# Kernel tuning notes

Hardware: AMD Instinct MI355X
Metric: run time of the kernel (lower is better)

The kernel has to match this reference:

```python
import jax, jax.numpy as jnp
import numpy as np

B, N, D, H, E = 4, 1024, 1024, 2048, 8

def setup_inputs() -> dict:
    key = jax.random.key(0)
    ks = jax.random.split(key, 5)
    return {
        "x": jax.random.normal(ks[0], (B, N, D), dtype=jnp.float32),
        "gate_w": jax.random.normal(ks[1], (D, E), dtype=jnp.float32) * 0.02,
        "gate_b": jnp.zeros((E,), dtype=jnp.float32),
        "w1": jax.random.normal(ks[2], (E, D, H), dtype=jnp.float32) * 0.02,
        "b1": jnp.zeros((E, H), dtype=jnp.float32),
        "w2": jax.random.normal(ks[3], (E, H, D), dtype=jnp.float32) * 0.02,
        "b2": jnp.zeros((E, D), dtype=jnp.float32),
        "gamma": jnp.ones((D,), dtype=jnp.float32),
    }

def reference(x, gate_w, gate_b, w1, b1, w2, b2, gamma):
    b, n, d = x.shape
    e = w1.shape[0]
    xf = x.reshape(b * n, d)                                    # [T, D]
    # gate: softmax over experts, then top-1
    probs = jax.nn.softmax(xf @ gate_w + gate_b, axis=-1)       # [T, E]
    top_val = jnp.max(probs, axis=-1, keepdims=True)            # [T, 1]
    top_idx = jnp.argmax(probs, axis=-1)                        # [T]
    # all-expert FFN (dense reference for masked dispatch; dropout in eval)
    h = jax.nn.gelu(jnp.einsum('td,edh->eth', xf, w1) + b1[:, None, :],
                    approximate=False)                          # [E, T, H]
    eo = jnp.einsum('eth,ehd->etd', h, w2) + b2[:, None, :]     # [E, T, D]
    onehot = jax.nn.one_hot(top_idx, e, dtype=xf.dtype)         # [T, E]
    out = jnp.einsum('etd,te->td', eo, onehot)                  # select routed expert
    y = (xf + out * top_val).reshape(b, n, d)
    # RMSNorm: F.normalize (L2, eps=1e-12) * gamma * sqrt(dim)
    nrm = jnp.linalg.norm(y, axis=-1, keepdims=True)
    y = y / jnp.maximum(nrm, 1e-12) * gamma * np.float32(np.sqrt(d))
    # load-balancing loss (unbiased variance like torch.var)
    importance = probs.sum(axis=0)                              # [E]
    load_loss = jnp.var(importance, ddof=1) / (jnp.mean(importance) ** 2 + 1e-10)
    return jax.nn.gelu(y, approximate=False), load_loss
```

## Files before the change

### kernel.cpp

```cpp
#include <hip/hip_runtime.h>
#include <math.h>

#define T_TOK 4096
#define DIM   1024
#define HID   2048
#define NE    8
#define TMM   128
#define BK    64
#define GATE_BLOCKS (T_TOK / 4)

typedef unsigned int  u32;
typedef unsigned short u16;
typedef __attribute__((ext_vector_type(8))) short bf16x8;
typedef __attribute__((ext_vector_type(8))) unsigned short u16x8;
typedef __attribute__((ext_vector_type(4))) float f32x4;

__device__ __forceinline__ float gelu_exact(float v) {
    return 0.5f * v * (1.0f + erff(v * 0.70710678118654752440f));
}

__device__ __forceinline__ float gelu_fast(float x) {
    float u = 1.5957691216057308f * (x + 0.044715f * x * x * x);
    float e = __expf(u);
    float t = 1.f - 2.f / (e + 1.f);
    return 0.5f * x * (1.f + t);
}

__device__ __forceinline__ u16 f2bf(float v) {
    u32 u = __float_as_uint(v);
    u32 r = (u + 0x7FFFu + ((u >> 16) & 1u)) >> 16;
    return (u16)r;
}

__device__ __forceinline__ void gld_lds16(const void* g, void* l) {
    __builtin_amdgcn_global_load_lds(
        (const __attribute__((address_space(1))) u32*)g,
        (__attribute__((address_space(3))) u32*)l,
        16, 0, 0);
}

__device__ __forceinline__ void transpose_body(
    const float* __restrict__ in, u16* __restrict__ out, int R, int C,
    int bx, int by, int bz, float (*tile)[65])
{
    const float* src = in  + (size_t)bz * R * C;
    u16*         dst = out + (size_t)bz * R * C;
    const int c0 = bx * 64, r0 = by * 64;
    const int th = threadIdx.x;

    const int tr  = th >> 4;
    const int tc4 = (th & 15) * 4;
    #pragma unroll
    for (int i = 0; i < 4; i++) {
        const int r = tr + i * 16;
        float4 v = *(const float4*)&src[(size_t)(r0 + r) * C + c0 + tc4];
        tile[r][tc4 + 0] = v.x; tile[r][tc4 + 1] = v.y;
        tile[r][tc4 + 2] = v.z; tile[r][tc4 + 3] = v.w;
    }
    __syncthreads();
    const int cc  = th >> 3;
    const int rr8 = (th & 7) * 8;
    #pragma unroll
    for (int i = 0; i < 2; i++) {
        const int c = cc + i * 32;
        u16x8 o;
        #pragma unroll
        for (int j = 0; j < 8; j++) o[j] = f2bf(tile[rr8 + j][c]);
        *(u16x8*)&dst[(size_t)(c0 + c) * R + r0 + rr8] = o;
    }
}

__global__ __launch_bounds__(256) void prep_kernel(
    const float* __restrict__ w1, const float* __restrict__ w2,
    u16* __restrict__ w1t, u16* __restrict__ w2t,
    const float* __restrict__ x, const float* __restrict__ gw,
    const float* __restrict__ gb, float* __restrict__ top_val,
    int* __restrict__ top_idx, float* __restrict__ partial_imp,
    int* __restrict__ partial_cnt)
{
    __shared__ float tile[64][65];
    __shared__ float s_imp[NE];
    __shared__ int   s_cnt[NE];

    const int id = blockIdx.x;
    if (id < 4096) {
        transpose_body(w1, w1t, DIM, HID, id & 31, (id >> 5) & 15, id >> 9, tile);
        return;
    }
    if (id < 8192) {
        const int i2 = id - 4096;
        transpose_body(w2, w2t, HID, DIM, i2 & 15, (i2 >> 4) & 31, i2 >> 9, tile);
        return;
    }

    const int g = id - 8192;
    const int th = threadIdx.x;
    if (th < NE) { s_imp[th] = 0.f; s_cnt[th] = 0; }
    __syncthreads();

    const int wave = th >> 6;
    const int lane = th & 63;
    const int t = g * 4 + wave;

    float acc[NE];
    #pragma unroll
    for (int e = 0; e < NE; e++) acc[e] = 0.f;

    const float* xr = x + (size_t)t * DIM;
    #pragma unroll 4
    for (int k = lane; k < DIM; k += 64) {
        float xv = xr[k];
        const float* gp = gw + (size_t)k * NE;
        float4 g0 = *(const float4*)gp;
        float4 g1 = *(const float4*)(gp + 4);
        acc[0] += xv * g0.x; acc[1] += xv * g0.y;
        acc[2] += xv * g0.z; acc[3] += xv * g0.w;
        acc[4] += xv * g1.x; acc[5] += xv * g1.y;
        acc[6] += xv * g1.z; acc[7] += xv * g1.w;
    }
    #pragma unroll
    for (int e = 0; e < NE; e++) {
        #pragma unroll
        for (int off = 32; off > 0; off >>= 1)
            acc[e] += __shfl_down(acc[e], off, 64);
    }
    if (lane == 0) {
        float l[NE];
        float m = -1e30f;
        #pragma unroll
        for (int e = 0; e < NE; e++) { l[e] = acc[e] + gb[e]; m = fmaxf(m, l[e]); }
        float s = 0.f;
        #pragma unroll
        for (int e = 0; e < NE; e++) { l[e] = expf(l[e] - m); s += l[e]; }
        float inv = 1.f / s;
        int bi = 0; float bv = -1.f;
        #pragma unroll
        for (int e = 0; e < NE; e++) {
            float p = l[e] * inv;
            atomicAdd(&s_imp[e], p);
            if (p > bv) { bv = p; bi = e; }
        }
        top_val[t] = bv;
        top_idx[t] = bi;
        atomicAdd(&s_cnt[bi], 1);
    }
    __syncthreads();
    if (th < NE) {
        partial_imp[g * NE + th] = s_imp[th];
        partial_cnt[g * NE + th] = s_cnt[th];
    }
}

__global__ __launch_bounds__(256) void route_kernel(
    const float* __restrict__ partial_imp, const int* __restrict__ partial_cnt,
    const int* __restrict__ top_idx,
    int* __restrict__ sorted_tok,
    int* __restrict__ tile_e, int* __restrict__ tile_s,
    int* __restrict__ tile_rows, int* __restrict__ ntiles,
    float* __restrict__ loss_out)
{
    __shared__ float rimp[32][NE];
    __shared__ int   rcnt[32][NE];
    __shared__ int   s_off[NE];
    __shared__ int   s_cur[NE];
    const int th = threadIdx.x;
    const int e = th & 7, chunk = th >> 3;
    float si = 0.f; int sc = 0;
    #pragma unroll 8
    for (int i = 0; i < GATE_BLOCKS / 32; i++) {
        const int b = chunk * (GATE_BLOCKS / 32) + i;
        si += partial_imp[b * NE + e];
        sc += partial_cnt[b * NE + e];
    }
    rimp[chunk][e] = si;
    rcnt[chunk][e] = sc;
    __syncthreads();
    if (th < NE) {
        float s = 0.f; int c = 0;
        for (int i = 0; i < 32; i++) { s += rimp[i][th]; c += rcnt[i][th]; }
        rimp[0][th] = s;
        rcnt[0][th] = c;
        s_cur[th] = 0;
    }
    __syncthreads();
    if (th == 0) {
        int off = 0, nt = 0;
        for (int ee = 0; ee < NE; ee++) {
            s_off[ee] = off;
            const int c = rcnt[0][ee];
            for (int s = 0; s < c; s += TMM) {
                tile_e[nt] = ee;
                tile_s[nt] = off + s;
                tile_rows[nt] = min(TMM, c - s);
                nt++;
            }
            off += c;
        }
        *ntiles = nt;

        float mean = 0.f;
        for (int ee = 0; ee < NE; ee++) mean += rimp[0][ee];
        mean *= (1.0f / NE);
        float var = 0.f;
        for (int ee = 0; ee < NE; ee++) { float d = rimp[0][ee] - mean; var += d * d; }
        var *= (1.0f / (NE - 1));
        loss_out[0] = var / (mean * mean + 1e-10f);
    }
    __syncthreads();
    #pragma unroll 4
    for (int r = 0; r < T_TOK / 256; r++) {
        const int t  = r * 256 + th;
        const int te = top_idx[t];
        const int rank = atomicAdd(&s_cur[te], 1);
        sorted_tok[s_off[te] + rank] = t;
    }
}

__global__ __launch_bounds__(256) void gather_x_kernel(
    const float* __restrict__ x, const int* __restrict__ sorted_tok,
    u16* __restrict__ xs)
{
    const int s = blockIdx.x;
    const int tok = sorted_tok[s];
    const float* src = x + (size_t)tok * DIM;
    u16* dst = xs + (size_t)s * DIM;
    const int i = threadIdx.x * 4;
    float4 v = *(const float4*)&src[i];
    ushort4 o;
    o.x = f2bf(v.x); o.y = f2bf(v.y); o.z = f2bf(v.z); o.w = f2bf(v.w);
    *(ushort4*)&dst[i] = o;
}

__global__ __launch_bounds__(512) void ffn1_mfma(
    const u16* __restrict__ xs, const u16* __restrict__ w1t,
    const float* __restrict__ b1,
    const int* __restrict__ tile_e, const int* __restrict__ tile_s,
    const int* __restrict__ tile_rows, const int* __restrict__ ntiles,
    u16* __restrict__ h_buf)
{
    const int tile = blockIdx.x;
    if (tile >= *ntiles) return;
    const int e     = tile_e[tile];
    const int sbase = tile_s[tile];
    const int rows  = tile_rows[tile];
    const int nbase = blockIdx.y * 256;

    __shared__ __align__(16) u16 As[128 * BK];
    __shared__ __align__(16) u16 Bs[256 * BK];

    const int th = threadIdx.x;
    const int w  = th >> 6;
    const int l  = th & 63;
    const int wm = w >> 2, wn = w & 3;
    const int lr = l >> 3;
    const int lcs = ((l & 7) ^ lr) * 8;

    const u16* aptr[2];
    #pragma unroll
    for (int c = 0; c < 2; c++) {
        int srow = sbase + c * 64 + w * 8 + lr;
        if (srow > T_TOK - 1) srow = T_TOK - 1;
        aptr[c] = xs + (size_t)srow * DIM + lcs;
    }
    const u16* wb = w1t + (size_t)e * HID * DIM + (size_t)nbase * DIM;
    const u16* bptr[4];
    #pragma unroll
    for (int c = 0; c < 4; c++)
        bptr[c] = wb + (size_t)(c * 64 + w * 8 + lr) * DIM + lcs;

    f32x4 acc[4][4] = {};

    for (int k0 = 0; k0 < DIM; k0 += BK) {
        __syncthreads();
        #pragma unroll
        for (int c = 0; c < 2; c++)
            gld_lds16(aptr[c] + k0, &As[(c * 64 + w * 8) * BK]);
        #pragma unroll
        for (int c = 0; c < 4; c++)
            gld_lds16(bptr[c] + k0, &Bs[(c * 64 + w * 8) * BK]);
        __syncthreads();
        #pragma unroll
        for (int ks = 0; ks < 2; ks++) {
            const int ko = ((ks * 4 + (l >> 4)) ^ (l & 7)) * 8;
            bf16x8 af[4], bfr[4];
            #pragma unroll
            for (int i = 0; i < 4; i++)
                af[i]  = *(const bf16x8*)&As[(wm * 64 + i * 16 + (l & 15)) * BK + ko];
            #pragma unroll
            for (int i = 0; i < 4; i++)
                bfr[i] = *(const bf16x8*)&Bs[(wn * 64 + i * 16 + (l & 15)) * BK + ko];
            #pragma unroll
            for (int mi = 0; mi < 4; mi++)
                #pragma unroll
                for (int ni = 0; ni < 4; ni++)
                    acc[mi][ni] = __builtin_amdgcn_mfma_f32_16x16x32_bf16(
                        af[mi], bfr[ni], acc[mi][ni], 0, 0, 0);
        }
    }

    const int col = l & 15, quad = l >> 4;
    #pragma unroll
    for (int ni = 0; ni < 4; ni++) {
        const int n = nbase + wn * 64 + ni * 16 + col;
        const float bias = b1[e * HID + n];
        #pragma unroll
        for (int mi = 0; mi < 4; mi++) {
            #pragma unroll
            for (int r = 0; r < 4; r++) {
                const int m = wm * 64 + mi * 16 + quad * 4 + r;
                if (m < rows) {
                    float v = acc[mi][ni][r] + bias;
                    h_buf[(size_t)(sbase + m) * HID + n] = f2bf(gelu_fast(v));
                }
            }
        }
    }
}

__global__ __launch_bounds__(256) void ffn2_mfma(
    const u16* __restrict__ h_buf, const u16* __restrict__ w2t,
    const float* __restrict__ b2, const float* __restrict__ x,
    const int* __restrict__ sorted_tok, const float* __restrict__ top_val,
    const int* __restrict__ tile_e, const int* __restrict__ tile_s,
    const int* __restrict__ tile_rows, const int* __restrict__ ntiles,
    float* __restrict__ yout)
{
    const int tile = blockIdx.x;
    if (tile >= *ntiles) return;
    const int e     = tile_e[tile];
    const int sbase = tile_s[tile];
    const int rows  = tile_rows[tile];
    const int nbase = blockIdx.y * 128;

    __shared__ __align__(16) u16 As[128 * BK];
    __shared__ __align__(16) u16 Bs[128 * BK];

    const int th = threadIdx.x;
    const int w  = th >> 6;
    const int l  = th & 63;
    const int wm = w >> 1, wn = w & 1;
    const int lr = l >> 3;
    const int lcs = ((l & 7) ^ lr) * 8;

    const u16* aptr[4];
    #pragma unroll
    for (int c = 0; c < 4; c++) {
        int srow = sbase + w * 32 + c * 8 + lr;
        if (srow > T_TOK - 1) srow = T_TOK - 1;
        aptr[c] = h_buf + (size_t)srow * HID + lcs;
    }
    const u16* wb = w2t + (size_t)e * DIM * HID + (size_t)nbase * HID;
    const u16* bptr[4];
    #pragma unroll
    for (int c = 0; c < 4; c++)
        bptr[c] = wb + (size_t)(w * 32 + c * 8 + lr) * HID + lcs;

    f32x4 acc[4][4] = {};

    for (int k0 = 0; k0 < HID; k0 += BK) {
        __syncthreads();
        #pragma unroll
        for (int c = 0; c < 4; c++)
            gld_lds16(aptr[c] + k0, &As[(w * 32 + c * 8) * BK]);
        #pragma unroll
        for (int c = 0; c < 4; c++)
            gld_lds16(bptr[c] + k0, &Bs[(w * 32 + c * 8) * BK]);
        __syncthreads();
        #pragma unroll
        for (int ks = 0; ks < 2; ks++) {
            const int ko = ((ks * 4 + (l >> 4)) ^ (l & 7)) * 8;
            bf16x8 af[4], bfr[4];
            #pragma unroll
            for (int i = 0; i < 4; i++)
                af[i]  = *(const bf16x8*)&As[(wm * 64 + i * 16 + (l & 15)) * BK + ko];
            #pragma unroll
            for (int i = 0; i < 4; i++)
                bfr[i] = *(const bf16x8*)&Bs[(wn * 64 + i * 16 + (l & 15)) * BK + ko];
            #pragma unroll
            for (int mi = 0; mi < 4; mi++)
                #pragma unroll
                for (int ni = 0; ni < 4; ni++)
                    acc[mi][ni] = __builtin_amdgcn_mfma_f32_16x16x32_bf16(
                        af[mi], bfr[ni], acc[mi][ni], 0, 0, 0);
        }
    }

    const int col = l & 15, quad = l >> 4;
    float bias[4];
    #pragma unroll
    for (int ni = 0; ni < 4; ni++)
        bias[ni] = b2[e * DIM + nbase + wn * 64 + ni * 16 + col];

    #pragma unroll
    for (int mi = 0; mi < 4; mi++) {
        #pragma unroll
        for (int r = 0; r < 4; r++) {
            const int m = wm * 64 + mi * 16 + quad * 4 + r;
            if (m < rows) {
                const int t = sorted_tok[sbase + m];
                const float tv = top_val[t];
                #pragma unroll
                for (int ni = 0; ni < 4; ni++) {
                    const int n = nbase + wn * 64 + ni * 16 + col;
                    float v = acc[mi][ni][r] + bias[ni];
                    yout[(size_t)t * DIM + n] = x[(size_t)t * DIM + n] + v * tv;
                }
            }
        }
    }
}

__global__ __launch_bounds__(256) void norm_kernel(float* __restrict__ y,
                                                   const float* __restrict__ gamma)
{
    const int t = blockIdx.x;
    float* row = y + (size_t)t * DIM;
    const int th = threadIdx.x;
    float4 v = *(const float4*)&row[th * 4];
    float ss = v.x * v.x + v.y * v.y + v.z * v.z + v.w * v.w;

    const int lane = th & 63, wave = th >> 6;
    #pragma unroll
    for (int off = 32; off > 0; off >>= 1) ss += __shfl_down(ss, off, 64);
    __shared__ float red[4];
    if (lane == 0) red[wave] = ss;
    __syncthreads();
    float total = red[0] + red[1] + red[2] + red[3];

    float nrm = sqrtf(total);
    float scale = 32.0f / fmaxf(nrm, 1e-12f);

    float4 g = *(const float4*)&gamma[th * 4];
    float4 o;
    o.x = gelu_exact(v.x * scale * g.x);
    o.y = gelu_exact(v.y * scale * g.y);
    o.z = gelu_exact(v.z * scale * g.z);
    o.w = gelu_exact(v.w * scale * g.w);
    *(float4*)&row[th * 4] = o;
}

extern "C" void kernel_launch(void* const* d_in, const int* in_sizes, int n_in,
                              void* d_out, int out_size, void* d_ws, size_t ws_size,
                              hipStream_t stream) {
    const float* x      = (const float*)d_in[0];
    const float* gate_w = (const float*)d_in[1];
    const float* gate_b = (const float*)d_in[2];
    const float* w1     = (const float*)d_in[3];
    const float* b1     = (const float*)d_in[4];
    const float* w2     = (const float*)d_in[5];
    const float* b2     = (const float*)d_in[6];
    const float* gamma  = (const float*)d_in[7];

    float* out  = (float*)d_out;
    float* loss = out + (size_t)T_TOK * DIM;

    char* ws = (char*)d_ws;
    float* top_val     = (float*)(ws + 0);
    int*   top_idx     = (int*)  (ws + 16384);
    int*   sorted_tok  = (int*)  (ws + 32768);
    int*   tile_e      = (int*)  (ws + 49664);
    int*   tile_s      = (int*)  (ws + 50176);
    int*   tile_rows   = (int*)  (ws + 50688);
    int*   ntiles      = (int*)  (ws + 51200);
    float* partial_imp = (float*)(ws + 65536);
    int*   partial_cnt = (int*)  (ws + 98304);
    u16*   x_sorted    = (u16*)  (ws + 131072);
    u16*   h_buf       = (u16*)  (ws + 131072 + 8388608);
    u16*   w1t         = (u16*)  (ws + 131072 + 8388608 + 16777216);
    u16*   w2t         = (u16*)  (ws + 131072 + 8388608 + 16777216 + 33554432);

    prep_kernel<<<8192 + GATE_BLOCKS, 256, 0, stream>>>(
        w1, w2, w1t, w2t, x, gate_w, gate_b, top_val, top_idx,
        partial_imp, partial_cnt);
    route_kernel<<<1, 256, 0, stream>>>(partial_imp, partial_cnt, top_idx,
                                        sorted_tok, tile_e, tile_s, tile_rows,
                                        ntiles, loss);
    gather_x_kernel<<<T_TOK, 256, 0, stream>>>(x, sorted_tok, x_sorted);

    ffn1_mfma<<<dim3(40, HID / 256), 512, 0, stream>>>(
        x_sorted, w1t, b1, tile_e, tile_s, tile_rows, ntiles, h_buf);
    ffn2_mfma<<<dim3(40, DIM / 128), 256, 0, stream>>>(
        h_buf, w2t, b2, x, sorted_tok, top_val, tile_e, tile_s, tile_rows,
        ntiles, out);
    norm_kernel<<<T_TOK, 256, 0, stream>>>(out, gamma);
}
```

Baseline: 301.7 us.

## Fuse bf16 x conversion into gate pass and gather rows indirectly in FFN1

Removes the separate gather_x kernel: the gate pass now writes a bf16 copy of x in token order, and FFN1 indexes rows through sorted_tok when issuing its LDS loads. Separately, each weight-transpose block now handles a 64x128 tile in two halves, halving the number of transpose blocks. This saves one launch and a full pass over x, but FFN1's A-tile loads become scattered row accesses, and the gate pass adds narrow per-lane 2-byte stores.

```diff
diff --git a/kernel.cpp b/kernel.cpp
--- a/kernel.cpp
+++ b/kernel.cpp
@@ -8,6 +8,7 @@
 #define TMM   128
 #define BK    64
 #define GATE_BLOCKS (T_TOK / 4)
+#define PREP_IDS (4096 + GATE_BLOCKS)
 
 typedef unsigned int  u32;
 typedef unsigned short u16;
@@ -39,34 +40,46 @@
         16, 0, 0);
 }
 
-__device__ __forceinline__ void transpose_body(
+__device__ __forceinline__ void transpose_body2(
     const float* __restrict__ in, u16* __restrict__ out, int R, int C,
     int bx, int by, int bz, float (*tile)[65])
 {
     const float* src = in  + (size_t)bz * R * C;
     u16*         dst = out + (size_t)bz * R * C;
-    const int c0 = bx * 64, r0 = by * 64;
+    const int c0 = bx * 128, r0 = by * 64;
     const int th = threadIdx.x;
 
     const int tr  = th >> 4;
     const int tc4 = (th & 15) * 4;
-    #pragma unroll
-    for (int i = 0; i < 4; i++) {
-        const int r = tr + i * 16;
-        float4 v = *(const float4*)&src[(size_t)(r0 + r) * C + c0 + tc4];
-        tile[r][tc4 + 0] = v.x; tile[r][tc4 + 1] = v.y;
-        tile[r][tc4 + 2] = v.z; tile[r][tc4 + 3] = v.w;
-    }
-    __syncthreads();
-    const int cc  = th >> 3;
-    const int rr8 = (th & 7) * 8;
-    #pragma unroll
-    for (int i = 0; i < 2; i++) {
-        const int c = cc + i * 32;
-        u16x8 o;
-        #pragma unroll
-        for (int j = 0; j < 8; j++) o[j] = f2bf(tile[rr8 + j][c]);
-        *(u16x8*)&dst[(size_t)(c0 + c) * R + r0 + rr8] = o;
+
+    float4 v[2][4];
+    #pragma unroll
+    for (int h = 0; h < 2; h++)
+        #pragma unroll
+        for (int i = 0; i < 4; i++)
+            v[h][i] = *(const float4*)&src[(size_t)(r0 + tr + i * 16) * C +
+                                           c0 + h * 64 + tc4];
+
+    #pragma unroll
+    for (int h = 0; h < 2; h++) {
+        if (h) __syncthreads();
+        #pragma unroll
+        for (int i = 0; i < 4; i++) {
+            const int r = tr + i * 16;
+            tile[r][tc4 + 0] = v[h][i].x; tile[r][tc4 + 1] = v[h][i].y;
+            tile[r][tc4 + 2] = v[h][i].z; tile[r][tc4 + 3] = v[h][i].w;
+        }
+        __syncthreads();
+        const int cc  = th >> 3;
+        const int rr8 = (th & 7) * 8;
+        #pragma unroll
+        for (int i = 0; i < 2; i++) {
+            const int c = cc + i * 32;
+            u16x8 o;
+            #pragma unroll
+            for (int j = 0; j < 8; j++) o[j] = f2bf(tile[rr8 + j][c]);
+            *(u16x8*)&dst[(size_t)(c0 + h * 64 + c) * R + r0 + rr8] = o;
+        }
     }
 }
 
@@ -74,26 +87,26 @@
     const float* __restrict__ w1, const float* __restrict__ w2,
     u16* __restrict__ w1t, u16* __restrict__ w2t,
     const float* __restrict__ x, const float* __restrict__ gw,
-    const float* __restrict__ gb, float* __restrict__ top_val,
-    int* __restrict__ top_idx, float* __restrict__ partial_imp,
-    int* __restrict__ partial_cnt)
+    const float* __restrict__ gb, u16* __restrict__ xbf,
+    float* __restrict__ top_val, int* __restrict__ top_idx,
+    float* __restrict__ partial_imp, int* __restrict__ partial_cnt)
 {
     __shared__ float tile[64][65];
     __shared__ float s_imp[NE];
     __shared__ int   s_cnt[NE];
 
     const int id = blockIdx.x;
+    if (id < 2048) {
+        transpose_body2(w1, w1t, DIM, HID, id & 15, (id >> 4) & 15, id >> 8, tile);
+        return;
+    }
     if (id < 4096) {
-        transpose_body(w1, w1t, DIM, HID, id & 31, (id >> 5) & 15, id >> 9, tile);
+        const int i2 = id - 2048;
+        transpose_body2(w2, w2t, HID, DIM, i2 & 7, (i2 >> 3) & 31, i2 >> 8, tile);
         return;
     }
-    if (id < 8192) {
-        const int i2 = id - 4096;
-        transpose_body(w2, w2t, HID, DIM, i2 & 15, (i2 >> 4) & 31, i2 >> 9, tile);
-        return;
-    }
-
-    const int g = id - 8192;
+
+    const int g = id - 4096;
     const int th = threadIdx.x;
     if (th < NE) { s_imp[th] = 0.f; s_cnt[th] = 0; }
     __syncthreads();
@@ -107,9 +120,11 @@
     for (int e = 0; e < NE; e++) acc[e] = 0.f;
 
     const float* xr = x + (size_t)t * DIM;
+    u16* xb = xbf + (size_t)t * DIM;
     #pragma unroll 4
     for (int k = lane; k < DIM; k += 64) {
         float xv = xr[k];
+        xb[k] = f2bf(xv);
         const float* gp = gw + (size_t)k * NE;
         float4 g0 = *(const float4*)gp;
         float4 g1 = *(const float4*)(gp + 4);
@@ -216,24 +231,9 @@
     }
 }
 
-__global__ __launch_bounds__(256) void gather_x_kernel(
-    const float* __restrict__ x, const int* __restrict__ sorted_tok,
-    u16* __restrict__ xs)
-{
-    const int s = blockIdx.x;
-    const int tok = sorted_tok[s];
-    const float* src = x + (size_t)tok * DIM;
-    u16* dst = xs + (size_t)s * DIM;
-    const int i = threadIdx.x * 4;
-    float4 v = *(const float4*)&src[i];
-    ushort4 o;
-    o.x = f2bf(v.x); o.y = f2bf(v.y); o.z = f2bf(v.z); o.w = f2bf(v.w);
-    *(ushort4*)&dst[i] = o;
-}
-
 __global__ __launch_bounds__(512) void ffn1_mfma(
-    const u16* __restrict__ xs, const u16* __restrict__ w1t,
-    const float* __restrict__ b1,
+    const u16* __restrict__ xbf, const u16* __restrict__ w1t,
+    const float* __restrict__ b1, const int* __restrict__ sorted_tok,
     const int* __restrict__ tile_e, const int* __restrict__ tile_s,
     const int* __restrict__ tile_rows, const int* __restrict__ ntiles,
     u16* __restrict__ h_buf)
@@ -260,7 +260,8 @@
     for (int c = 0; c < 2; c++) {
         int srow = sbase + c * 64 + w * 8 + lr;
         if (srow > T_TOK - 1) srow = T_TOK - 1;
-        aptr[c] = xs + (size_t)srow * DIM + lcs;
+        const int tok = sorted_tok[srow];
+        aptr[c] = xbf + (size_t)tok * DIM + lcs;
     }
     const u16* wb = w1t + (size_t)e * HID * DIM + (size_t)nbase * DIM;
     const u16* bptr[4];
@@ -464,21 +465,20 @@
     int*   ntiles      = (int*)  (ws + 51200);
     float* partial_imp = (float*)(ws + 65536);
     int*   partial_cnt = (int*)  (ws + 98304);
-    u16*   x_sorted    = (u16*)  (ws + 131072);
+    u16*   xbf         = (u16*)  (ws + 131072);
     u16*   h_buf       = (u16*)  (ws + 131072 + 8388608);
     u16*   w1t         = (u16*)  (ws + 131072 + 8388608 + 16777216);
     u16*   w2t         = (u16*)  (ws + 131072 + 8388608 + 16777216 + 33554432);
 
-    prep_kernel<<<8192 + GATE_BLOCKS, 256, 0, stream>>>(
-        w1, w2, w1t, w2t, x, gate_w, gate_b, top_val, top_idx,
+    prep_kernel<<<PREP_IDS, 256, 0, stream>>>(
+        w1, w2, w1t, w2t, x, gate_w, gate_b, xbf, top_val, top_idx,
         partial_imp, partial_cnt);
     route_kernel<<<1, 256, 0, stream>>>(partial_imp, partial_cnt, top_idx,
                                         sorted_tok, tile_e, tile_s, tile_rows,
                                         ntiles, loss);
-    gather_x_kernel<<<T_TOK, 256, 0, stream>>>(x, sorted_tok, x_sorted);
 
     ffn1_mfma<<<dim3(40, HID / 256), 512, 0, stream>>>(
-        x_sorted, w1t, b1, tile_e, tile_s, tile_rows, ntiles, h_buf);
+        xbf, w1t, b1, sorted_tok, tile_e, tile_s, tile_rows, ntiles, h_buf);
     ffn2_mfma<<<dim3(40, DIM / 128), 256, 0, stream>>>(
         h_buf, w2t, b2, x, sorted_tok, top_val, tile_e, tile_s, tile_rows,
         ntiles, out);
```

New measurement: 296.2 us. About the same (-1.8%).
